# Kernel tuning notes

Hardware: AMD Instinct MI355X
Metric: run time of the kernel (lower is better)

## Reference

```python
import jax, jax.numpy as jnp
import numpy as np

B, N, C, H = 2, 2048, 768, 12
D = C // H
EPS = 1e-5


def setup_inputs() -> dict:
    key = jax.random.key(0)
    ks = jax.random.split(key, 12)
    s = 0.02
    return {
        "x": jax.random.normal(ks[0], (B, N, C), jnp.float32),
        "attn_mask": jax.random.randint(ks[1], (N, N), 0, 2) > 0,  # True = NOT allowed
        "ln1_g": jnp.ones((C,), jnp.float32),
        "ln1_b": jnp.zeros((C,), jnp.float32),
        "w_qkv": jax.random.normal(ks[2], (C, 3 * C), jnp.float32) * s,  # [in,out]
        "b_qkv": jnp.zeros((3 * C,), jnp.float32),
        "w_proj": jax.random.normal(ks[3], (C, C), jnp.float32) * s,
        "b_proj": jnp.zeros((C,), jnp.float32),
        "ls1": jnp.full((C,), 1e-5, jnp.float32),
        "ln2_g": jnp.ones((C,), jnp.float32),
        "ln2_b": jnp.zeros((C,), jnp.float32),
        "w1": jax.random.normal(ks[4], (C, 4 * C), jnp.float32) * s,
        "b1": jnp.zeros((4 * C,), jnp.float32),
        "w2": jax.random.normal(ks[5], (4 * C, C), jnp.float32) * s,
        "b2": jnp.zeros((C,), jnp.float32),
        "ls2": jnp.full((C,), 1e-5, jnp.float32),
    }


def layer_norm(x, g, b):
    mu = jnp.mean(x, axis=-1, keepdims=True)
    var = jnp.var(x, axis=-1, keepdims=True)
    return (x - mu) * jax.lax.rsqrt(var + EPS) * g + b


def reference(x, attn_mask, ln1_g, ln1_b, w_qkv, b_qkv, w_proj, b_proj, ls1,
              ln2_g, ln2_b, w1, b1, w2, b2, ls2):
    # ---- attention branch ----
    h = layer_norm(x, ln1_g, ln1_b)
    qkv = h @ w_qkv + b_qkv                       # [B,N,3C]
    qkv = qkv.reshape(B, N, 3, H, D).transpose(2, 0, 3, 1, 4)  # [3,B,H,N,D]
    q, k, v = qkv[0], qkv[1], qkv[2]
    scores = jnp.einsum('bhnd,bhmd->bhnm', q, k) * (D ** -0.5)  # [B,H,N,N]
    neg = jnp.finfo(scores.dtype).min
    scores = jnp.where(attn_mask, neg, scores)    # mask broadcasts over B,H
    attn = jax.nn.softmax(scores, axis=-1)
    o = jnp.einsum('bhnm,bhmd->bhnd', attn, v).transpose(0, 2, 1, 3).reshape(B, N, C)
    x = x + (o @ w_proj + b_proj) * ls1
    # ---- MLP branch ----
    h = layer_norm(x, ln2_g, ln2_b)
    h = jax.nn.gelu(h @ w1 + b1, approximate=False)
    x = x + (h @ w2 + b2) * ls2
    return x
```

## Files before the change

kernel.cpp:

```cpp
#include <hip/hip_runtime.h>
#include <hip/hip_bf16.h>
#include <math.h>

#define BN 2
#define SEQ 2048
#define CH 768
#define NH 12
#define HD 64
#define TOK (BN*SEQ)


using bf16_t = __hip_bfloat16;
typedef __attribute__((ext_vector_type(8))) short short8;
typedef __attribute__((ext_vector_type(8))) unsigned short ushort8;
typedef __attribute__((ext_vector_type(4))) float floatx4;
typedef __attribute__((ext_vector_type(2))) unsigned uintx2;

#define OFF_LN1G 0
#define OFF_LN1B 768
#define OFF_BQKV 1536
#define OFF_BPROJ 3840
#define OFF_LS1 4608
#define OFF_LN2G 5376
#define OFF_LN2B 6144
#define OFF_B1 6912
#define OFF_B2 9984
#define OFF_LS2 10752

__device__ inline float b2f(bf16_t v){ return __bfloat162float(v); }
__device__ inline bf16_t f2b(float v){ return __float2bfloat16(v); }
__device__ inline short f2bs(float v){ bf16_t b = __float2bfloat16(v); return *reinterpret_cast<short*>(&b); }
__device__ inline unsigned pk2(float a, float b){
  return (unsigned)(unsigned short)f2bs(a) | ((unsigned)(unsigned short)f2bs(b) << 16);
}
__device__ inline unsigned cvtpk(float a, float b){
  unsigned r;
  asm("v_cvt_pk_bf16_f32 %0, %1, %2" : "=v"(r) : "v"(a), "v"(b));
  return r;
}
__device__ inline float sane(float v){ return (fabsf(v) < 1e30f) ? v : 0.0f; }
__device__ inline float clampf(float v, float lim){
  v = sane(v);
  return fminf(fmaxf(v, -lim), lim);
}
__device__ inline float ldf(const bf16_t* p){ return __bfloat162float(*p); }
__device__ inline float ldf(const float* p){ return *p; }
__device__ inline bool bf16_mode(const void* gref){
  return *reinterpret_cast<const unsigned*>(gref) == 0x3F803F80u;
}
__device__ inline void gload16(const void* g, void* l){
  __builtin_amdgcn_global_load_lds(
      (const __attribute__((address_space(1))) unsigned int*)g,
      (__attribute__((address_space(3))) unsigned int*)l, 16, 0, 0);
}

template<typename T>
__device__ inline void tr32(const T* __restrict__ src, size_t colOff, int stride,
    bf16_t* __restrict__ dst, int dstStride, int r0, int c0, float* smem, int tid)
{
  const int tx = tid & 31, ty = tid >> 5;
  #pragma unroll
  for (int j = 0; j < 4; j++)
    smem[(ty + j*8)*33 + tx] = ldf(src + (size_t)(r0 + ty + j*8) * stride + colOff + c0 + tx);
  __syncthreads();
  #pragma unroll
  for (int j = 0; j < 4; j++)
    dst[(size_t)(c0 + ty + j*8) * dstStride + r0 + tx] = f2b(smem[tx*33 + ty + j*8]);
}

template<typename T, bool GUARDED>
__global__ __launch_bounds__(256) void prep1_kernel(
    const T* __restrict__ x, const T* __restrict__ w_qkv, const T* __restrict__ w_proj,
    const T* __restrict__ w1, const T* __restrict__ w2,
    const T* __restrict__ g1, const T* __restrict__ b1_, const T* __restrict__ bqkv,
    const T* __restrict__ bproj, const T* __restrict__ ls1, const T* __restrict__ g2,
    const T* __restrict__ b2_, const T* __restrict__ bb1, const T* __restrict__ bb2,
    const T* __restrict__ ls2, const void* __restrict__ mask,
    float* __restrict__ pb, bf16_t* __restrict__ wqkvT, bf16_t* __restrict__ wprojT,
    unsigned long long* __restrict__ m1, bf16_t* __restrict__ a1,
    bf16_t* __restrict__ w1T, bf16_t* __restrict__ w2T,
    const void* __restrict__ gref)
{
  if (GUARDED && (bf16_mode(gref) != (sizeof(T) == 2))) return;
  __shared__ float smem[1056];
  const int tid = threadIdx.x;
  int wg = blockIdx.x;

  if (wg < 4096) {
    const T* xr = x + (size_t)wg * CH;
    float v0 = sane(ldf(xr + tid)), v1 = sane(ldf(xr + tid + 256)), v2 = sane(ldf(xr + tid + 512));
    float s  = v0 + v1 + v2;
    float s2 = v0*v0 + v1*v1 + v2*v2;
    #pragma unroll
    for (int o = 32; o > 0; o >>= 1) { s += __shfl_down(s, o, 64); s2 += __shfl_down(s2, o, 64); }
    if ((tid & 63) == 0) { smem[tid >> 6] = s; smem[(tid >> 6) + 4] = s2; }
    __syncthreads();
    if (tid == 0) {
      float ts = smem[0] + smem[1] + smem[2] + smem[3];
      float tq = smem[4] + smem[5] + smem[6] + smem[7];
      float mu = ts * (1.f / CH);
      float var = tq * (1.f / CH) - mu * mu;
      smem[8] = mu; smem[9] = rsqrtf(fmaxf(var, 0.f) + 1e-5f);
    }
    __syncthreads();
    const float mu = smem[8], rs = smem[9];
    bf16_t* orow = a1 + (size_t)wg * CH;
    orow[tid      ] = f2b(clampf((v0 - mu) * rs * ldf(g1 + tid      ) + ldf(b1_ + tid      ), 32.f));
    orow[tid + 256] = f2b(clampf((v1 - mu) * rs * ldf(g1 + tid + 256) + ldf(b1_ + tid + 256), 32.f));
    orow[tid + 512] = f2b(clampf((v2 - mu) * rs * ldf(g1 + tid + 512) + ldf(b1_ + tid + 512), 32.f));
    return;
  }
  wg -= 4096;
  if (wg < 1728) {
    tr32(w_qkv, 0, 2304, wqkvT, 768, (wg / 72) * 32, (wg % 72) * 32, smem, tid);
    return;
  }
  wg -= 1728;
  if (wg < 576) {
    tr32(w_proj, 0, 768, wprojT, 768, (wg / 24) * 32, (wg % 24) * 32, smem, tid);
    return;
  }
  wg -= 576;
  if (wg < 512) {
    const unsigned* mw = (const unsigned*)mask;
    unsigned accu = 0;
    #pragma unroll 8
    for (int i = 0; i < 64; i++) accu |= mw[i];
    const bool is8 = (accu > 1u);
    const int wave = tid >> 6, lane = tid & 63;
    #pragma unroll 4
    for (int i = 0; i < 32; i++) {
      const int word = wg * 128 + wave * 32 + i;
      const size_t elem = (size_t)word * 64 + lane;
      bool pred;
      if (is8) pred = ((const unsigned char*)mask)[elem] != 0;
      else     pred = ((const int*)mask)[elem] != 0;
      unsigned long long bits = __ballot(pred);
      if (lane == 0) m1[word] = bits;
    }
    return;
  }
  wg -= 512;
  if (wg < 1) {
    #define PCOPY(off, src, n) for (int i = tid; i < (n); i += 256) pb[(off)+i] = ldf((src)+i);
    PCOPY(OFF_LN1G, g1, 768)
    PCOPY(OFF_LN1B, b1_, 768)
    PCOPY(OFF_BQKV, bqkv, 2304)
    PCOPY(OFF_BPROJ, bproj, 768)
    PCOPY(OFF_LS1, ls1, 768)
    PCOPY(OFF_LN2G, g2, 768)
    PCOPY(OFF_LN2B, b2_, 768)
    PCOPY(OFF_B1, bb1, 3072)
    PCOPY(OFF_B2, bb2, 768)
    PCOPY(OFF_LS2, ls2, 768)
    #undef PCOPY
    return;
  }
  wg -= 1;
  if (wg < 2304) {
    tr32(w1, 0, 3072, w1T, 768, (wg / 96) * 32, (wg % 96) * 32, smem, tid);
    return;
  }
  wg -= 2304;
  {
    tr32(w2, 0, 768, w2T, 3072, (wg / 24) * 32, (wg % 24) * 32, smem, tid);
    return;
  }
}

template<typename T, bool GUARDED>
__global__ __launch_bounds__(256) void trc_kernel(const T* __restrict__ w1,
    const T* __restrict__ w2, bf16_t* __restrict__ w1Tc, bf16_t* __restrict__ w2Tc,
    int kc, const void* __restrict__ gref)
{
  if (GUARDED && (bf16_mode(gref) != (sizeof(T) == 2))) return;
  __shared__ float smem[1056];
  const int tid = threadIdx.x;
  int wg = blockIdx.x;
  if (wg < 576) {
    tr32(w1, (size_t)kc * 768, 3072, w1Tc, 768, (wg / 24) * 32, (wg % 24) * 32, smem, tid);
  } else {
    wg -= 576;
    tr32(w2 + (size_t)kc * 768 * 768, 0, 768, w2Tc, 768, (wg / 24) * 32, (wg % 24) * 32, smem, tid);
  }
}

__global__ __launch_bounds__(256) void ln2x_kernel(const bf16_t* __restrict__ x1,
    bf16_t* __restrict__ a2, const float* __restrict__ pb)
{
  __shared__ float red[10];
  const int row = blockIdx.x, tid = threadIdx.x;
  const bf16_t* xr = x1 + (size_t)row * CH;
  float v0 = sane(ldf(xr + tid)), v1 = sane(ldf(xr + tid + 256)), v2 = sane(ldf(xr + tid + 512));
  float s  = v0 + v1 + v2;
  float s2 = v0*v0 + v1*v1 + v2*v2;
  #pragma unroll
  for (int o = 32; o > 0; o >>= 1) { s += __shfl_down(s, o, 64); s2 += __shfl_down(s2, o, 64); }
  if ((tid & 63) == 0) { red[tid >> 6] = s; red[(tid >> 6) + 4] = s2; }
  __syncthreads();
  if (tid == 0) {
    float ts = red[0] + red[1] + red[2] + red[3];
    float tq = red[4] + red[5] + red[6] + red[7];
    float mu = ts * (1.f / CH);
    float var = tq * (1.f / CH) - mu * mu;
    red[8] = mu; red[9] = rsqrtf(fmaxf(var, 0.f) + 1e-5f);
  }
  __syncthreads();
  const float mu = red[8], rs = red[9];
  bf16_t* orow = a2 + (size_t)row * CH;
  orow[tid      ] = f2b(clampf((v0 - mu) * rs * pb[OFF_LN2G + tid      ] + pb[OFF_LN2B + tid      ], 32.f));
  orow[tid + 256] = f2b(clampf((v1 - mu) * rs * pb[OFF_LN2G + tid + 256] + pb[OFF_LN2B + tid + 256], 32.f));
  orow[tid + 512] = f2b(clampf((v2 - mu) * rs * pb[OFF_LN2G + tid + 512] + pb[OFF_LN2B + tid + 512], 32.f));
}

template<int MODE, int MT, int NT, int KS>
__global__ __launch_bounds__(256) void mgemm(
    const bf16_t* __restrict__ A, const bf16_t* __restrict__ BT,
    const float* __restrict__ pb, const int K, const int ldb,
    const int biasOff, const int scaleOff,
    const void* __restrict__ resid, const void* __restrict__ gref,
    bf16_t* __restrict__ o0, bf16_t* __restrict__ o1, bf16_t* __restrict__ vtout,
    float* __restrict__ oF, const bf16_t* __restrict__ stg,
    const int addPrev, const int finalize)
{
  constexpr int MI = MT / 32;
  constexpr int NI = NT / 32;
  constexpr int SH = KS / 32;
  static_assert(MT * KS == 4096 && NT * KS == 4096, "LDS sizing");
  __shared__ __align__(16) short As[2][4096];
  __shared__ __align__(16) short Bs[2][4096];
  const int tid = threadIdx.x;
  const int wave = tid >> 6, lane = tid & 63, lane15 = lane & 15, quad = lane >> 4;
  const int wr = (wave >> 1) * (MT / 2), wc = (wave & 1) * (NT / 2);

  int bflat = blockIdx.y * gridDim.x + blockIdx.x;
  const int nwg = gridDim.x * gridDim.y;
  bflat = (bflat & 7) * (nwg >> 3) + (bflat >> 3);
  const int bX = bflat % gridDim.x, bY = bflat / gridDim.x;
  const int mBase = bY * MT;
  const int nBase = bX * NT;

  floatx4 acc[MI][NI];
  #pragma unroll
  for (int mi = 0; mi < MI; mi++)
    #pragma unroll
    for (int ni = 0; ni < NI; ni++) acc[mi][ni] = (floatx4){0.f, 0.f, 0.f, 0.f};

  const bf16_t* aS0 = A  + (size_t)(mBase + (tid >> 2)) * K + (tid & 3) * 8;
  const bf16_t* aS1 = aS0 + (size_t)64 * K;
  const bf16_t* bS0 = BT + (size_t)(nBase + (tid >> 2)) * ldb + (tid & 3) * 8;
  const bf16_t* bS1 = bS0 + (size_t)64 * ldb;
  const int wfl = __builtin_amdgcn_readfirstlane(wave);
  short* aB = &As[0][0];
  short* bB = &Bs[0][0];

  auto STAGE = [&](int buf, int k0) {
    if (KS == 32) {
      gload16(aS0 + k0, aB + buf * 4096 + wfl * 512);
      if (MT == 128) gload16(aS1 + k0, aB + buf * 4096 + 2048 + wfl * 512);
      gload16(bS0 + k0, bB + buf * 4096 + wfl * 512);
      if (NT == 128) gload16(bS1 + k0, bB + buf * 4096 + 2048 + wfl * 512);
    } else {
      #pragma unroll
      for (int s = 0; s < 2; s++) {
        gload16(aS0 + k0 + s * 32, aB + buf * 4096 + s * 2048 + wfl * 512);
        gload16(bS0 + k0 + s * 32, bB + buf * 4096 + s * 2048 + wfl * 512);
      }
    }
  };

  const int nsteps = K / KS;
  int cur = 0;
  STAGE(0, 0);
  asm volatile("s_waitcnt vmcnt(0)" ::: "memory");
  __builtin_amdgcn_s_barrier();
  for (int t = 0; t < nsteps; ++t) {
    if (t + 1 < nsteps) STAGE(cur ^ 1, (t + 1) * KS);
    #pragma unroll
    for (int s = 0; s < SH; s++) {
      short8 av[MI], bv[NI];
      #pragma unroll
      for (int mi = 0; mi < MI; mi++)
        av[mi] = *(const short8*)&As[cur][s * 2048 + (wr + mi * 16 + lane15) * 32 + quad * 8];
      #pragma unroll
      for (int ni = 0; ni < NI; ni++)
        bv[ni] = *(const short8*)&Bs[cur][s * 2048 + (wc + ni * 16 + lane15) * 32 + quad * 8];
      #pragma unroll
      for (int mi = 0; mi < MI; mi++)
        #pragma unroll
        for (int ni = 0; ni < NI; ni++)
          acc[mi][ni] = __builtin_amdgcn_mfma_f32_16x16x32_bf16(av[mi], bv[ni], acc[mi][ni], 0, 0, 0);
    }
    if (t + 1 < nsteps) {
      asm volatile("s_waitcnt vmcnt(0)" ::: "memory");
      __builtin_amdgcn_s_barrier();
      cur ^= 1;
    }
  }

  const bool rbf = (MODE == 1) ? bf16_mode(gref) : false;
  #pragma unroll
  for (int mi = 0; mi < MI; mi++) {
    #pragma unroll
    for (int ni = 0; ni < NI; ni++) {
      const int c0u = nBase + wc + ni * 16;
      const int col = c0u + lane15;
      float bia = 0.f, sc = 0.f;
      if (MODE == 0 || MODE == 1 || MODE == 2) bia = pb[biasOff + col];
      if (MODE == 1) sc = pb[scaleOff + col];
      if (MODE == 3 && finalize) { bia = pb[biasOff + col]; sc = pb[scaleOff + col]; }
      if (MODE == 0 && c0u >= 2 * CH) {
        const int cv = col - 2 * CH;
        const int bh = (mBase >> 11) * NH + (cv >> 6);
        const int d = cv & 63;
        const int tok0 = (mBase + wr + mi * 16 + quad * 4) & (SEQ - 1);
        float tv[4];
        #pragma unroll
        for (int r = 0; r < 4; r++) tv[r] = clampf(acc[mi][ni][r] + bia, 20.f);
        uintx2 pk = (uintx2){ pk2(tv[0], tv[1]), pk2(tv[2], tv[3]) };
        *(uintx2*)(vtout + ((size_t)(bh * 64 + d)) * SEQ + tok0) = pk;
        continue;
      }
      #pragma unroll
      for (int r = 0; r < 4; r++) {
        const int row = mBase + wr + mi * 16 + quad * 4 + r;
        float v = acc[mi][ni][r];
        if (MODE == 0) {
          const float cv = clampf(v + bia, 20.f);
          if (col < CH) o0[(size_t)row * CH + col] = f2b(cv * 0.125f);
          else          o1[(size_t)row * CH + (col - CH)] = f2b(cv);
        } else if (MODE == 1) {
          const size_t ix = (size_t)row * CH + col;
          const float rx = rbf ? b2f(((const bf16_t*)resid)[ix]) : ((const float*)resid)[ix];
          const bf16_t xv = f2b(rx + clampf(sc * (v + bia), 0.5f));
          o0[ix] = xv;
          o1[ix] = xv;
        } else if (MODE == 2) {
          const float h = v + bia;
          const float g = 0.5f * h * (1.f + erff(h * 0.70710678118f));
          o0[(size_t)row * CH + col] = f2b(clampf(g, 50.f));
        } else {
          const size_t ix = (size_t)row * CH + col;
          if (addPrev) v += oF[ix];
          if (!finalize) oF[ix] = v;
          else oF[ix] = b2f(stg[ix]) + clampf(sc * (v + bia), 0.5f);
        }
      }
    }
  }
}

__global__ __launch_bounds__(256) void attn9_kernel(bf16_t* __restrict__ q,
    const bf16_t* __restrict__ kbuf, const bf16_t* __restrict__ vtb,
    const unsigned long long* __restrict__ m1)
{
  __shared__ __align__(16) short Ks[2][64 * 72];
  __shared__ __align__(16) short Vs[2][64 * 72];
  __shared__ unsigned Plds[4][32 * 17];
  const int iflat = blockIdx.y * 32 + blockIdx.x;
  const int bh = (iflat & 7) * 3 + ((iflat >> 3) >> 5);
  const int q0 = ((iflat >> 3) & 31) * 64;
  const int b = bh / NH, h = bh % NH;
  const int tid = threadIdx.x;
  const int wave = tid >> 6, l15 = tid & 15, quad = (tid & 63) >> 4;
  const int srow = tid >> 2, scc = (tid & 3) * 16;
  const size_t kgbase = (size_t)(b * SEQ) * CH + h * HD;
  const size_t vgbase = (size_t)(bh * HD) * SEQ;
  const int qrow = q0 + wave * 16 + l15;

  short8 qf[2];
  {
    const unsigned short* qp = (const unsigned short*)q
        + (size_t)(b * SEQ + qrow) * CH + h * HD + quad * 8;
    qf[0] = *(const short8*)(qp);
    qf[1] = *(const short8*)(qp + 32);
  }
  const unsigned long long* mrow = m1 + (size_t)qrow * (SEQ / 64);

  float mreg = -1.1e4f, lreg = 0.f;
  floatx4 oacc[4] = {{0,0,0,0},{0,0,0,0},{0,0,0,0},{0,0,0,0}};
  unsigned* pw = &Plds[wave][0];

  const unsigned short* kp0 = (const unsigned short*)kbuf + kgbase + (size_t)srow * CH + scc;
  const unsigned short* vp0 = (const unsigned short*)vtb + vgbase + (size_t)srow * SEQ + scc;

  {
    ushort8 k0r = *(const ushort8*)(kp0);
    ushort8 k1r = *(const ushort8*)(kp0 + 8);
    ushort8 v0r = *(const ushort8*)(vp0);
    ushort8 v1r = *(const ushort8*)(vp0 + 8);
    *(ushort8*)&Ks[0][srow * 72 + scc]     = k0r;
    *(ushort8*)&Ks[0][srow * 72 + scc + 8] = k1r;
    *(ushort8*)&Vs[0][srow * 72 + scc]     = v0r;
    *(ushort8*)&Vs[0][srow * 72 + scc + 8] = v1r;
  }
  __syncthreads();

  int cur = 0;
  ushort8 kr0, kr1, vr0, vr1;
  for (int k0 = 0; k0 < SEQ; k0 += 64) {
    const bool more = (k0 + 64 < SEQ);
    if (more) {
      const unsigned short* kp = kp0 + (size_t)(k0 + 64) * CH;
      const unsigned short* vp = vp0 + (k0 + 64);
      kr0 = *(const ushort8*)(kp);
      kr1 = *(const ushort8*)(kp + 8);
      vr0 = *(const ushort8*)(vp);
      vr1 = *(const ushort8*)(vp + 8);
    }

    const unsigned long long mw = mrow[k0 >> 6];
    float sv[4][4];
    float kbm[4];
    #pragma unroll
    for (int kb = 0; kb < 4; kb++) {
      floatx4 t = {0,0,0,0};
      short8 kf0 = *(const short8*)&Ks[cur][(kb * 16 + l15) * 72 + quad * 8];
      short8 kf1 = *(const short8*)&Ks[cur][(kb * 16 + l15) * 72 + 32 + quad * 8];
      __builtin_amdgcn_s_setprio(1);
      t = __builtin_amdgcn_mfma_f32_16x16x32_bf16(kf0, qf[0], t, 0, 0, 0);
      t = __builtin_amdgcn_mfma_f32_16x16x32_bf16(kf1, qf[1], t, 0, 0, 0);
      __builtin_amdgcn_s_setprio(0);
      #pragma unroll
      for (int r = 0; r < 4; r++) {
        float v = t[r];
        if ((mw >> (kb * 16 + quad * 4 + r)) & 1ull) v = -1.0e30f;
        sv[kb][r] = v;
      }
      kbm[kb] = fmaxf(fmaxf(fmaxf(sv[kb][0], sv[kb][1]), sv[kb][2]), sv[kb][3]);
    }
    float tmax = fmaxf(fmaxf(fmaxf(kbm[0], kbm[1]), kbm[2]), kbm[3]);
    tmax = fmaxf(tmax, __shfl_xor(tmax, 16, 64));
    tmax = fmaxf(tmax, __shfl_xor(tmax, 32, 64));

    if (__any(tmax > mreg)) {
      const float mnew = fmaxf(mreg, tmax);
      float alpha = __expf(mreg - mnew);
      alpha = (alpha <= 1.f) ? alpha : 0.f;
      lreg *= alpha;
      #pragma unroll
      for (int db = 0; db < 4; db++)
        #pragma unroll
        for (int r = 0; r < 4; r++) oacc[db][r] *= alpha;
      mreg = mnew;
    }

    float ls = 0.f;
    #pragma unroll
    for (int kb = 0; kb < 4; kb++) {
      float pr[4];
      #pragma unroll
      for (int r = 0; r < 4; r++) {
        const float pv = __expf(sv[kb][r] - mreg);
        pr[r] = pv;
        ls += pv;
      }
      pw[(8 * kb + 2 * quad)     * 17 + l15] = cvtpk(pr[0], pr[1]);
      pw[(8 * kb + 2 * quad + 1) * 17 + l15] = cvtpk(pr[2], pr[3]);
    }
    ls += __shfl_xor(ls, 16, 64);
    ls += __shfl_xor(ls, 32, 64);
    lreg += ls;

    #pragma unroll
    for (int s = 0; s < 2; s++) {
      union { unsigned u[4]; short8 s8; } pu;
      #pragma unroll
      for (int w = 0; w < 4; w++)
        pu.u[w] = pw[(16 * s + 4 * quad + w) * 17 + l15];
      __builtin_amdgcn_s_setprio(1);
      #pragma unroll
      for (int db = 0; db < 4; db++) {
        short8 vf = *(const short8*)&Vs[cur][(db * 16 + l15) * 72 + s * 32 + quad * 8];
        oacc[db] = __builtin_amdgcn_mfma_f32_16x16x32_bf16(vf, pu.s8, oacc[db], 0, 0, 0);
      }
      __builtin_amdgcn_s_setprio(0);
    }

    if (more) {
      *(ushort8*)&Ks[cur ^ 1][srow * 72 + scc]     = kr0;
      *(ushort8*)&Ks[cur ^ 1][srow * 72 + scc + 8] = kr1;
      *(ushort8*)&Vs[cur ^ 1][srow * 72 + scc]     = vr0;
      *(ushort8*)&Vs[cur ^ 1][srow * 72 + scc + 8] = vr1;
      __syncthreads();
      cur ^= 1;
    }
  }

  const float inv = 1.f / fmaxf(lreg, 1e-20f);
  unsigned short* op = (unsigned short*)q
      + (size_t)(b * SEQ + qrow) * CH + h * HD + quad * 4;
  #pragma unroll
  for (int db = 0; db < 4; db++) {
    const unsigned lo = pk2(clampf(oacc[db][0] * inv, 10.f), clampf(oacc[db][1] * inv, 10.f));
    const unsigned hi = pk2(clampf(oacc[db][2] * inv, 10.f), clampf(oacc[db][3] * inv, 10.f));
    *(uintx2*)(op + db * 16) = (uintx2){lo, hi};
  }
}

extern "C" void kernel_launch(void* const* d_in, const int* in_sizes, int n_in,
                              void* d_out, int out_size, void* d_ws, size_t ws_size,
                              hipStream_t stream) {
  const void* x      = d_in[0];
  const void* mask   = d_in[1];
  const void* ln1_g  = d_in[2];
  const void* ln1_b  = d_in[3];
  const void* w_qkv  = d_in[4];
  const void* b_qkv  = d_in[5];
  const void* w_proj = d_in[6];
  const void* b_proj = d_in[7];
  const void* ls1    = d_in[8];
  const void* ln2_g  = d_in[9];
  const void* ln2_b  = d_in[10];
  const void* w1     = d_in[11];
  const void* b1     = d_in[12];
  const void* w2     = d_in[13];
  const void* b2     = d_in[14];
  const void* ls2    = d_in[15];
  const void* gref   = ln1_g;

  char* ws = (char*)d_ws;
  float*  pb     = (float*)ws;
  bf16_t* a12    = (bf16_t*)(ws + 65536);
  bf16_t* vt     = (bf16_t*)(ws + 65536 + 6291456);
  bf16_t* stage  = vt;
  char*   r3     = ws + 65536 + 2 * 6291456;
  bf16_t* wqkvT  = (bf16_t*)r3;
  bf16_t* wprojT = (bf16_t*)(r3 + 3538944);
  unsigned long long* mi1 = (unsigned long long*)(r3 + 4718592);
  bf16_t* hact   = (bf16_t*)r3;
  char*   r4     = ws + 65536 + 3 * 6291456;
  bf16_t* w1Tc   = (bf16_t*)r4;
  bf16_t* w2Tc   = (bf16_t*)(r4 + 1179648);
  bf16_t* w1T    = (bf16_t*)r4;
  bf16_t* w2T    = (bf16_t*)(r4 + 4718592);
  bf16_t* dQ     = (bf16_t*)d_out;
  bf16_t* dK     = dQ + 3145728;
  float*  outF   = (float*)d_out;

  const long long xs = in_sizes ? (long long)in_sizes[0] : 0;
  const int mode = (xs == 6291456LL) ? 1 : (xs == 12582912LL ? 2 : 0);
  const bool doFull = (ws_size >= 28377088ULL);
  const int prepGrid = doFull ? 11521 : 6913;

  #define PREP_ARGS(T) (const T*)x, (const T*)w_qkv, (const T*)w_proj, (const T*)w1, (const T*)w2, \
      (const T*)ln1_g, (const T*)ln1_b, (const T*)b_qkv, (const T*)b_proj, (const T*)ls1, \
      (const T*)ln2_g, (const T*)ln2_b, (const T*)b1, (const T*)b2, (const T*)ls2, \
      mask, pb, wqkvT, wprojT, mi1, a12, w1T, w2T, gref
  if (mode == 1)      prep1_kernel<bf16_t, false><<<prepGrid, 256, 0, stream>>>(PREP_ARGS(bf16_t));
  else if (mode == 2) prep1_kernel<float,  false><<<prepGrid, 256, 0, stream>>>(PREP_ARGS(float));
  else {
    prep1_kernel<bf16_t, true><<<prepGrid, 256, 0, stream>>>(PREP_ARGS(bf16_t));
    prep1_kernel<float,  true><<<prepGrid, 256, 0, stream>>>(PREP_ARGS(float));
  }
  #undef PREP_ARGS

  mgemm<0, 128, 128, 32><<<dim3(18, 32), 256, 0, stream>>>(a12, wqkvT, pb, 768, 768, OFF_BQKV, 0,
      nullptr, gref, dQ, dK, vt, nullptr, nullptr, 0, 0);
  attn9_kernel<<<dim3(SEQ / 64, BN * NH), 256, 0, stream>>>(dQ, dK, vt, mi1);
  mgemm<1, 64, 64, 64><<<dim3(12, 64), 256, 0, stream>>>(dQ, wprojT, pb, 768, 768, OFF_BPROJ, OFF_LS1,
      x, gref, dK, stage, nullptr, nullptr, nullptr, 0, 0);
  ln2x_kernel<<<TOK, 256, 0, stream>>>(dK, a12, pb);
  for (int kc = 0; kc < 4; kc++) {
    const bf16_t* bt1; const bf16_t* bt2; int ldb2;
    if (doFull) {
      bt1 = w1T + (size_t)kc * 768 * 768;
      bt2 = w2T + (size_t)kc * 768;
      ldb2 = 3072;
    } else {
      if (mode == 1)      trc_kernel<bf16_t, false><<<1152, 256, 0, stream>>>((const bf16_t*)w1, (const bf16_t*)w2, w1Tc, w2Tc, kc, gref);
      else if (mode == 2) trc_kernel<float,  false><<<1152, 256, 0, stream>>>((const float*)w1,  (const float*)w2,  w1Tc, w2Tc, kc, gref);
      else {
        trc_kernel<bf16_t, true><<<1152, 256, 0, stream>>>((const bf16_t*)w1, (const bf16_t*)w2, w1Tc, w2Tc, kc, gref);
        trc_kernel<float,  true><<<1152, 256, 0, stream>>>((const float*)w1,  (const float*)w2,  w1Tc, w2Tc, kc, gref);
      }
      bt1 = w1Tc; bt2 = w2Tc; ldb2 = 768;
    }
    mgemm<2, 64, 64, 64><<<dim3(12, 64), 256, 0, stream>>>(a12, bt1, pb, 768, 768, OFF_B1 + kc * 768, 0,
        nullptr, gref, hact, nullptr, nullptr, nullptr, nullptr, 0, 0);
    mgemm<3, 64, 64, 64><<<dim3(12, 64), 256, 0, stream>>>(hact, bt2, pb, 768, ldb2, OFF_B2, OFF_LS2,
        nullptr, gref, nullptr, nullptr, nullptr, outF, stage, kc > 0 ? 1 : 0, kc == 3 ? 1 : 0);
  }
}
```

Before: 371.1 us.

## Chunk MLP over rows instead of hidden dim; retile QKV GEMM to 64x128

The MLP path with full workspace now splits the token dimension into four row chunks of 1024. Each chunk computes the full 3072-wide hidden activation and then the down-projection with K=3072 in a single pass. This replaces the four hidden-dim chunks that accumulated fp32 partial outputs through global read-modify-write. The QKV GEMM switches from 128x128x32 tiles to 64x128x64 tiles with twice as many workgroups, and the mgemm LDS and staging logic is generalized to arbitrary tile sizes. The trade-off is a larger hidden buffer per chunk and more B-matrix rereads across row chunks.

```diff
diff --git a/kernel.cpp b/kernel.cpp
--- a/kernel.cpp
+++ b/kernel.cpp
@@ -216,7 +216,7 @@
 template<int MODE, int MT, int NT, int KS>
 __global__ __launch_bounds__(256) void mgemm(
     const bf16_t* __restrict__ A, const bf16_t* __restrict__ BT,
-    const float* __restrict__ pb, const int K, const int ldb,
+    const float* __restrict__ pb, const int K, const int ldb, const int ldo,
     const int biasOff, const int scaleOff,
     const void* __restrict__ resid, const void* __restrict__ gref,
     bf16_t* __restrict__ o0, bf16_t* __restrict__ o1, bf16_t* __restrict__ vtout,
@@ -226,9 +226,10 @@
   constexpr int MI = MT / 32;
   constexpr int NI = NT / 32;
   constexpr int SH = KS / 32;
-  static_assert(MT * KS == 4096 && NT * KS == 4096, "LDS sizing");
-  __shared__ __align__(16) short As[2][4096];
-  __shared__ __align__(16) short Bs[2][4096];
+  constexpr int ASZ = MT * KS;
+  constexpr int BSZ = NT * KS;
+  __shared__ __align__(16) short As[2][ASZ];
+  __shared__ __align__(16) short Bs[2][BSZ];
   const int tid = threadIdx.x;
   const int wave = tid >> 6, lane = tid & 63, lane15 = lane & 15, quad = lane >> 4;
   const int wr = (wave >> 1) * (MT / 2), wc = (wave & 1) * (NT / 2);
@@ -255,17 +256,12 @@
   short* bB = &Bs[0][0];
 
   auto STAGE = [&](int buf, int k0) {
-    if (KS == 32) {
-      gload16(aS0 + k0, aB + buf * 4096 + wfl * 512);
-      if (MT == 128) gload16(aS1 + k0, aB + buf * 4096 + 2048 + wfl * 512);
-      gload16(bS0 + k0, bB + buf * 4096 + wfl * 512);
-      if (NT == 128) gload16(bS1 + k0, bB + buf * 4096 + 2048 + wfl * 512);
-    } else {
-      #pragma unroll
-      for (int s = 0; s < 2; s++) {
-        gload16(aS0 + k0 + s * 32, aB + buf * 4096 + s * 2048 + wfl * 512);
-        gload16(bS0 + k0 + s * 32, bB + buf * 4096 + s * 2048 + wfl * 512);
-      }
+    #pragma unroll
+    for (int s = 0; s < SH; s++) {
+      gload16(aS0 + k0 + s * 32, aB + buf * ASZ + s * (MT * 32) + wfl * 512);
+      if (MT == 128) gload16(aS1 + k0 + s * 32, aB + buf * ASZ + s * (MT * 32) + 2048 + wfl * 512);
+      gload16(bS0 + k0 + s * 32, bB + buf * BSZ + s * (NT * 32) + wfl * 512);
+      if (NT == 128) gload16(bS1 + k0 + s * 32, bB + buf * BSZ + s * (NT * 32) + 2048 + wfl * 512);
     }
   };
 
@@ -281,10 +277,10 @@
       short8 av[MI], bv[NI];
       #pragma unroll
       for (int mi = 0; mi < MI; mi++)
-        av[mi] = *(const short8*)&As[cur][s * 2048 + (wr + mi * 16 + lane15) * 32 + quad * 8];
+        av[mi] = *(const short8*)&As[cur][s * (MT * 32) + (wr + mi * 16 + lane15) * 32 + quad * 8];
       #pragma unroll
       for (int ni = 0; ni < NI; ni++)
-        bv[ni] = *(const short8*)&Bs[cur][s * 2048 + (wc + ni * 16 + lane15) * 32 + quad * 8];
+        bv[ni] = *(const short8*)&Bs[cur][s * (NT * 32) + (wc + ni * 16 + lane15) * 32 + quad * 8];
       #pragma unroll
       for (int mi = 0; mi < MI; mi++)
         #pragma unroll
@@ -338,7 +334,7 @@
         } else if (MODE == 2) {
           const float h = v + bia;
           const float g = 0.5f * h * (1.f + erff(h * 0.70710678118f));
-          o0[(size_t)row * CH + col] = f2b(clampf(g, 50.f));
+          o0[(size_t)row * ldo + col] = f2b(clampf(g, 50.f));
         } else {
           const size_t ix = (size_t)row * CH + col;
           if (addPrev) v += oF[ix];
@@ -555,30 +551,35 @@
   }
   #undef PREP_ARGS
 
-  mgemm<0, 128, 128, 32><<<dim3(18, 32), 256, 0, stream>>>(a12, wqkvT, pb, 768, 768, OFF_BQKV, 0,
-      nullptr, gref, dQ, dK, vt, nullptr, nullptr, 0, 0);
+  mgemm<0, 64, 128, 64><<<dim3(18, 64), 256, 0, stream>>>(a12, wqkvT, pb, 768, 768, 0,
+      OFF_BQKV, 0, nullptr, gref, dQ, dK, vt, nullptr, nullptr, 0, 0);
   attn9_kernel<<<dim3(SEQ / 64, BN * NH), 256, 0, stream>>>(dQ, dK, vt, mi1);
-  mgemm<1, 64, 64, 64><<<dim3(12, 64), 256, 0, stream>>>(dQ, wprojT, pb, 768, 768, OFF_BPROJ, OFF_LS1,
-      x, gref, dK, stage, nullptr, nullptr, nullptr, 0, 0);
+  mgemm<1, 64, 64, 64><<<dim3(12, 64), 256, 0, stream>>>(dQ, wprojT, pb, 768, 768, 0,
+      OFF_BPROJ, OFF_LS1, x, gref, dK, stage, nullptr, nullptr, nullptr, 0, 0);
   ln2x_kernel<<<TOK, 256, 0, stream>>>(dK, a12, pb);
-  for (int kc = 0; kc < 4; kc++) {
-    const bf16_t* bt1; const bf16_t* bt2; int ldb2;
-    if (doFull) {
-      bt1 = w1T + (size_t)kc * 768 * 768;
-      bt2 = w2T + (size_t)kc * 768;
-      ldb2 = 3072;
-    } else {
+  if (doFull) {
+    for (int mc = 0; mc < 4; mc++) {
+      const int ro = mc * 1024;
+      mgemm<2, 64, 64, 64><<<dim3(48, 16), 256, 0, stream>>>(a12 + (size_t)ro * CH, w1T,
+          pb, 768, 768, 3072, OFF_B1, 0, nullptr, gref, hact, nullptr, nullptr,
+          nullptr, nullptr, 0, 0);
+      mgemm<3, 64, 64, 64><<<dim3(12, 16), 256, 0, stream>>>(hact, w2T,
+          pb, 3072, 3072, 0, OFF_B2, OFF_LS2, nullptr, gref, nullptr, nullptr, nullptr,
+          outF + (size_t)ro * CH, stage + (size_t)ro * CH, 0, 1);
+    }
+  } else {
+    for (int kc = 0; kc < 4; kc++) {
       if (mode == 1)      trc_kernel<bf16_t, false><<<1152, 256, 0, stream>>>((const bf16_t*)w1, (const bf16_t*)w2, w1Tc, w2Tc, kc, gref);
       else if (mode == 2) trc_kernel<float,  false><<<1152, 256, 0, stream>>>((const float*)w1,  (const float*)w2,  w1Tc, w2Tc, kc, gref);
       else {
         trc_kernel<bf16_t, true><<<1152, 256, 0, stream>>>((const bf16_t*)w1, (const bf16_t*)w2, w1Tc, w2Tc, kc, gref);
         trc_kernel<float,  true><<<1152, 256, 0, stream>>>((const float*)w1,  (const float*)w2,  w1Tc, w2Tc, kc, gref);
       }
-      bt1 = w1Tc; bt2 = w2Tc; ldb2 = 768;
-    }
-    mgemm<2, 64, 64, 64><<<dim3(12, 64), 256, 0, stream>>>(a12, bt1, pb, 768, 768, OFF_B1 + kc * 768, 0,
-        nullptr, gref, hact, nullptr, nullptr, nullptr, nullptr, 0, 0);
-    mgemm<3, 64, 64, 64><<<dim3(12, 64), 256, 0, stream>>>(hact, bt2, pb, 768, ldb2, OFF_B2, OFF_LS2,
-        nullptr, gref, nullptr, nullptr, nullptr, outF, stage, kc > 0 ? 1 : 0, kc == 3 ? 1 : 0);
-  }
-}
+      mgemm<2, 64, 64, 64><<<dim3(12, 64), 256, 0, stream>>>(a12, w1Tc, pb, 768, 768, 768,
+          OFF_B1 + kc * 768, 0, nullptr, gref, hact, nullptr, nullptr, nullptr, nullptr, 0, 0);
+      mgemm<3, 64, 64, 64><<<dim3(12, 64), 256, 0, stream>>>(hact, w2Tc, pb, 768, 768, 0,
+          OFF_B2, OFF_LS2, nullptr, gref, nullptr, nullptr, nullptr, outF, stage,
+          kc > 0 ? 1 : 0, kc == 3 ? 1 : 0);
+    }
+  }
+}
```

Result: slower. 452.2 us (+21.9%).
